# Kernel optimization log

Measured on AMD Instinct MI355X. Metric: run time of the kernel, lower is better.

Reference implementation:

```python
import jax, jax.numpy as jnp
import numpy as np

N = 100000; E = 200000; H = 64; P2 = 250000; P3 = 500000; G = 2048; NC = 10
NF = 18; EF = 18; Y = 0.25; EPS_BN = 1e-5


def setup_inputs() -> dict:
    key = jax.random.key(0)
    ks = jax.random.split(key, 20)
    def rn(i, shape, s=0.05):
        return jax.random.normal(ks[i], shape, jnp.float32) * s
    inp = {}
    inp["x"] = jax.random.normal(ks[0], (N, NF), jnp.float32)
    inp["edge_attr"] = jax.random.normal(ks[1], (E, EF), jnp.float32)
    inp["paths2"] = jax.random.randint(ks[2], (P2, 2), 0, N, jnp.int32)
    inp["ei2"] = jax.random.randint(ks[3], (P2, 1), 0, E, jnp.int32)
    inp["paths3"] = jax.random.randint(ks[4], (P3, 3), 0, N, jnp.int32)
    inp["ei3"] = jax.random.randint(ks[5], (P3, 2), 0, E, jnp.int32)
    inp["batch"] = jnp.sort(jax.random.randint(ks[6], (N,), 0, G, jnp.int32))
    inp["w_feat"] = rn(7, (NF, H)); inp["b_feat"] = jnp.zeros((H,), jnp.float32)
    inp["w_bond"] = rn(8, (EF, H)); inp["b_bond"] = jnp.zeros((H,), jnp.float32)
    inp["w_ih"] = rn(9, (4 * H, 2 * H)); inp["w_hh"] = rn(10, (4 * H, H))
    inp["b_ih"] = jnp.zeros((4 * H,), jnp.float32); inp["b_hh"] = jnp.zeros((4 * H,), jnp.float32)
    inp["bn_g"] = jnp.ones((2, H), jnp.float32); inp["bn_b"] = jnp.zeros((2, H), jnp.float32)
    inp["mlp_w1"] = rn(11, (2, H, H)); inp["mlp_b1"] = jnp.zeros((2, H), jnp.float32)
    inp["bn1_g"] = jnp.ones((2, H), jnp.float32); inp["bn1_b"] = jnp.zeros((2, H), jnp.float32)
    inp["mlp_w2"] = rn(12, (2, H, H)); inp["mlp_b2"] = jnp.zeros((2, H), jnp.float32)
    inp["bn2_g"] = jnp.ones((2, H), jnp.float32); inp["bn2_b"] = jnp.zeros((2, H), jnp.float32)
    inp["w_att"] = rn(13, (H,)); inp["b_att"] = jnp.zeros((1,), jnp.float32)
    inp["w_l1"] = rn(14, (H, H)); inp["b_l1"] = jnp.zeros((H,), jnp.float32)
    inp["w_l2"] = rn(15, (H, NC)); inp["b_l2"] = jnp.zeros((NC,), jnp.float32)
    return inp


def _batch_norm(x, g, b):
    # training-mode BN: biased batch statistics, eps=1e-5 (torch BatchNorm1d)
    m = x.mean(axis=0)
    v = x.var(axis=0)
    return (x - m) * jax.lax.rsqrt(v + EPS_BN) * g + b


def _lstm_final(x_seq, w_ih, w_hh, b_ih, b_hh):
    # x_seq: [P, L, 2H]; torch LSTM gate order i,f,g,o; return final hidden [P, H]
    P = x_seq.shape[0]
    Hd = w_hh.shape[1]
    def step(carry, xt):
        h, c = carry
        gates = xt @ w_ih.T + b_ih + h @ w_hh.T + b_hh
        i, f, g, o = jnp.split(gates, 4, axis=-1)
        c = jax.nn.sigmoid(f) * c + jax.nn.sigmoid(i) * jnp.tanh(g)
        h = jax.nn.sigmoid(o) * jnp.tanh(c)
        return (h, c), None
    h0 = jnp.zeros((P, Hd), x_seq.dtype)
    (h, _), _ = jax.lax.scan(step, (h0, h0), jnp.swapaxes(x_seq, 0, 1))
    return h


def _conv(i, x_in, ea_enc, paths, ei, w_ih, w_hh, b_ih, b_hh, bn_g, bn_b,
          mlp_w1, mlp_b1, bn1_g, bn1_b, mlp_w2, mlp_b2, bn2_g, bn2_b):
    P = paths.shape[0]
    ea = ea_enc[ei]                                        # [P, L-1, H]
    ea = jnp.concatenate([jnp.zeros((P, 1, H), ea.dtype), ea], axis=1)  # [P, L, H]
    x_cat = jnp.concatenate([x_in[paths], ea], axis=-1)    # [P, L, 2H]
    h = _lstm_final(x_cat, w_ih, w_hh, b_ih, b_hh)         # [P, H]
    h = jax.ops.segment_sum(h, paths[:, -1], num_segments=N)  # scatter_add to nodes
    h = _batch_norm(h, bn_g[i], bn_b[i])                   # residuals=False
    h = jax.nn.relu(_batch_norm(h @ mlp_w1[i] + mlp_b1[i], bn1_g[i], bn1_b[i]))
    h = jax.nn.relu(_batch_norm(h @ mlp_w2[i] + mlp_b2[i], bn2_g[i], bn2_b[i]))
    return h


def _attention(query, keys, w_att, b_att):
    scores = []
    for k in keys:
        s = jnp.sum(query * k, axis=0)                     # [H], sum over nodes
        s = (s - s.min()) / (s.max() - s.min() + 1e-6)
        scores.append(s @ w_att + b_att[0])                # scalar
    w = jax.nn.softmax(jnp.stack(scores))                  # [K]
    rep = sum(k * w[j] for j, k in enumerate(keys))
    return rep + query


def _forward(x, edge_attr, w_feat, b_feat, w_bond, b_bond, w_ih, w_hh, b_ih, b_hh,
             bn_g, bn_b, mlp_w1, mlp_b1, bn1_g, bn1_b, mlp_w2, mlp_b2, bn2_g, bn2_b,
             w_att, b_att, w_l1, b_l1, w_l2, b_l2, paths2, ei2, paths3, ei3, batch):
    W0 = x @ w_feat + b_feat                               # [N, H]
    ea_enc = edge_attr @ w_bond + b_bond                   # [E, H]
    common = (w_ih, w_hh, b_ih, b_hh, bn_g, bn_b, mlp_w1, mlp_b1, bn1_g, bn1_b,
              mlp_w2, mlp_b2, bn2_g, bn2_b)
    W1 = _conv(0, W0, ea_enc, paths2, ei2, *common)
    Win = (1.0 - Y) * W0 - Y * W1
    W2 = _conv(1, Win, ea_enc, paths3, ei3, *common)
    out = _attention(W0, [W1, W2], w_att, b_att)           # [N, H]
    out = jax.ops.segment_sum(out, batch, num_segments=G)  # global_add_pool -> [G, H]
    out = jax.nn.relu(out @ w_l1 + b_l1)
    return out @ w_l2 + b_l2                               # [G, NC]


def reference(x, edge_attr, paths2, ei2, paths3, ei3, batch, w_feat, b_feat,
              w_bond, b_bond, w_ih, w_hh, b_ih, b_hh, bn_g, bn_b, mlp_w1, mlp_b1,
              bn1_g, bn1_b, mlp_w2, mlp_b2, bn2_g, bn2_b, w_att, b_att,
              w_l1, b_l1, w_l2, b_l2):
    return _forward(x, edge_attr, w_feat, b_feat, w_bond, b_bond, w_ih, w_hh, b_ih, b_hh,
                    bn_g, bn_b, mlp_w1, mlp_b1, bn1_g, bn1_b, mlp_w2, mlp_b2, bn2_g, bn2_b,
                    w_att, b_att, w_l1, b_l1, w_l2, b_l2, paths2, ei2, paths3, ei3, batch)
```

## Files before the change

### kernel.cpp

```cpp
#include <hip/hip_runtime.h>
#include <math.h>

#define NNODES 100000
#define NEDGES 200000
#define HD 64
#define NP2 250000
#define NP3 500000
#define NG 2048
#define NCLS 10
#define NFEAT 18
#define EFEAT 18

typedef short short8v __attribute__((ext_vector_type(8)));
typedef float f32x4 __attribute__((ext_vector_type(4)));

__device__ __forceinline__ unsigned short bf16r(float a) {
    unsigned u = __builtin_bit_cast(unsigned, a);
    return (unsigned short)((u + 0x7FFFu + ((u >> 16) & 1u)) >> 16);
}

__global__ void prep_bias(const float* __restrict__ b_ih, const float* __restrict__ b_hh,
                          float* __restrict__ bsum) {
    int j = threadIdx.x;
    bsum[j] = b_ih[j] + b_hh[j];
}

__global__ void prep_bp(const float* __restrict__ w_ih, const float* __restrict__ w_hh,
                        unsigned short* __restrict__ Bp) {
    int gid = blockIdx.x * 256 + threadIdx.x;
    if (gid >= 6 * 16 * 64 * 8) return;
    int kc = gid >> 13;
    int rem = gid & 8191;
    int nt = rem >> 9;
    int rem2 = rem & 511;
    int l = rem2 >> 3, j = rem2 & 7;
    int c = l & 15, q = l >> 4;
    int jh = nt >> 2, qg = nt & 3;
    int k = kc * 32 + q * 8 + j;
    int n = qg * 64 + 16 * jh + c;
    float f = (k < 128) ? w_ih[n * 128 + k] : w_hh[n * 64 + (k - 128)];
    Bp[gid] = bf16r(f);
}

__global__ void encode_all(const float* __restrict__ X, const float* __restrict__ Wf,
                           const float* __restrict__ bf,
                           const float* __restrict__ Ea, const float* __restrict__ Wb,
                           const float* __restrict__ bb,
                           float* __restrict__ W0, unsigned short* __restrict__ W0b,
                           unsigned short* __restrict__ eab) {
    long gid = (long)blockIdx.x * 256 + threadIdx.x;
    if (gid >= (long)(NNODES + NEDGES) * 64) return;
    long r = gid >> 6;
    int col = (int)(gid & 63);
    if (r < NNODES) {
        float acc = bf[col];
        const float* xr = X + r * NFEAT;
        for (int k = 0; k < NFEAT; ++k) acc += xr[k] * Wf[k * 64 + col];
        W0[gid] = acc;
        W0b[gid] = bf16r(acc);
    } else {
        long r2 = r - NNODES;
        float acc = bb[col];
        const float* xr = Ea + r2 * EFEAT;
        for (int k = 0; k < EFEAT; ++k) acc += xr[k] * Wb[k * 64 + col];
        eab[r2 * 64 + col] = bf16r(acc);
    }
}

template <int L>
__global__ __launch_bounds__(256, 2)
void conv_mfma(const unsigned short* __restrict__ xb, const unsigned short* __restrict__ eab,
               const int* __restrict__ paths, const int* __restrict__ ei,
               const unsigned short* __restrict__ Bp, const float* __restrict__ bsum,
               float* __restrict__ hsum, int P) {
    __shared__ unsigned short Al[64 * 200];

    const int t = threadIdx.x;
    const int w = t >> 6, lane = t & 63;
    const int c = lane & 15, q = lane >> 4;
    const int pl = t >> 2, gq = t & 3;
    const long pg = (long)blockIdx.x * 64 + pl;
    const int pc = (pg < P) ? (int)pg : P - 1;

    short8v Bfr[6][4];
#pragma unroll
    for (int kc = 0; kc < 6; ++kc)
#pragma unroll
        for (int qg = 0; qg < 4; ++qg)
            Bfr[kc][qg] = *(const short8v*)&Bp[(((kc * 16) + (w * 4 + qg)) * 64 + lane) * 8];

    float breg[4];
#pragma unroll
    for (int qg = 0; qg < 4; ++qg) breg[qg] = bsum[qg * 64 + 16 * w + c];

    float creg[16];
#pragma unroll
    for (int i = 0; i < 16; ++i) creg[i] = 0.f;

    f32x4 acc[4][4];

    uint4 nu0, nu1, ev0, ev1;
    {
        int node = paths[pc * L + 0];
        const uint4* s4 = (const uint4*)(xb + (size_t)node * HD);
        nu0 = s4[2 * gq]; nu1 = s4[2 * gq + 1];
    }

    for (int step = 0; step < L; ++step) {
        *(uint4*)&Al[pl * 200 + gq * 16] = nu0;
        *(uint4*)&Al[pl * 200 + gq * 16 + 8] = nu1;
        if (step > 0) {
            *(uint4*)&Al[pl * 200 + 64 + gq * 16] = ev0;
            *(uint4*)&Al[pl * 200 + 64 + gq * 16 + 8] = ev1;
        }
#pragma unroll
        for (int mt = 0; mt < 4; ++mt)
#pragma unroll
            for (int qg = 0; qg < 4; ++qg) {
                f32x4 v; v[0] = breg[qg]; v[1] = breg[qg]; v[2] = breg[qg]; v[3] = breg[qg];
                acc[mt][qg] = v;
            }
        __syncthreads();

        if (step + 1 < L) {
            int node = paths[pc * L + step + 1];
            const uint4* s4 = (const uint4*)(xb + (size_t)node * HD);
            nu0 = s4[2 * gq]; nu1 = s4[2 * gq + 1];
            int e = ei[pc * (L - 1) + step];
            const uint4* e4 = (const uint4*)(eab + (size_t)e * HD);
            ev0 = e4[2 * gq]; ev1 = e4[2 * gq + 1];
        }

#define CHUNK(KC)                                                              \
        {                                                                      \
            _Pragma("unroll")                                                  \
            for (int mt = 0; mt < 4; ++mt) {                                   \
                short8v af = *(const short8v*)&Al[(mt * 16 + c) * 200 + (KC) * 32 + q * 8]; \
                _Pragma("unroll")                                              \
                for (int qg = 0; qg < 4; ++qg)                                 \
                    acc[mt][qg] = __builtin_amdgcn_mfma_f32_16x16x32_bf16(     \
                        af, Bfr[KC][qg], acc[mt][qg], 0, 0, 0);                \
            }                                                                  \
        }
        if (step == 0) {
            CHUNK(0) CHUNK(1)
        } else {
            CHUNK(0) CHUNK(1) CHUNK(2) CHUNK(3) CHUNK(4) CHUNK(5)
        }
#undef CHUNK
        __syncthreads();

#pragma unroll
        for (int mt = 0; mt < 4; ++mt) {
#pragma unroll
            for (int r = 0; r < 4; ++r) {
                float gi = acc[mt][0][r], gf = acc[mt][1][r];
                float gg = acc[mt][2][r], go = acc[mt][3][r];
                float ea = __expf(-gf), eb = __expf(-gi);
                float ed = __expf(-2.f * gg), eo = __expf(-go);
                float pa = 1.f + ea, pb = 1.f + eb, pd = 1.f + ed;
                float cn = (creg[mt * 4 + r] * pb * pd + (1.f - ed) * pa) *
                           __builtin_amdgcn_rcpf(pa * pb * pd);
                creg[mt * 4 + r] = cn;
                float et = __expf(-2.f * cn);
                float hn = (1.f - et) *
                           __builtin_amdgcn_rcpf((1.f + eo) * (1.f + et));
                if (step < L - 1) {
                    Al[(mt * 16 + q * 4 + r) * 200 + 128 + 16 * w + c] = bf16r(hn);
                } else {
                    long pr = (long)blockIdx.x * 64 + mt * 16 + q * 4 + r;
                    if (pr < P) {
                        int node = paths[pr * L + (L - 1)];
                        atomicAdd(hsum + (size_t)node * HD + 16 * w + c, hn);
                    }
                }
            }
        }
    }
}

__global__ void col_stats(const float* __restrict__ X, int nrows, float* __restrict__ out) {
    int col = threadIdx.x & 63, rg = threadIdx.x >> 6;
    float s = 0.f, q = 0.f;
    long stride = (long)gridDim.x * 4;
    for (long r = (long)blockIdx.x * 4 + rg; r < nrows; r += stride) {
        float v = X[r * 64 + col];
        s += v;
        q += v * v;
    }
    __shared__ float red[2][256];
    red[0][threadIdx.x] = s;
    red[1][threadIdx.x] = q;
    __syncthreads();
    if (threadIdx.x < 64) {
        int c = threadIdx.x;
        float ss = red[0][c] + red[0][c + 64] + red[0][c + 128] + red[0][c + 192];
        float qq = red[1][c] + red[1][c + 64] + red[1][c + 128] + red[1][c + 192];
        atomicAdd(out + c, ss);
        atomicAdd(out + 64 + c, qq);
    }
}

__device__ __forceinline__ void bn_affine(const float* stats, const float* g,
                                          const float* b, int col, int nrows,
                                          float& a, float& c) {
    float inv = 1.0f / (float)nrows;
    float mean = stats[col] * inv;
    float var = stats[64 + col] * inv - mean * mean;
    a = g[col] * rsqrtf(var + 1e-5f);
    c = b[col] - mean * a;
}

template <bool INRELU, bool STATS>
__global__ __launch_bounds__(256)
void gemm64(const float* __restrict__ X, const float* __restrict__ stats_in,
            const float* __restrict__ bn_gm, const float* __restrict__ bn_bt,
            const float* __restrict__ W, const float* __restrict__ bias,
            float* __restrict__ Y, float* stats, int nrows) {
    __shared__ float Xs[64 * 64];
    __shared__ float red[2][256];
    const int t = threadIdx.x;
    const int col = t & 63, rg = t >> 6;
    const long r0 = (long)blockIdx.x * 64;

    float a = 1.f, c = 0.f;
    if (stats_in) bn_affine(stats_in, bn_gm, bn_bt, col, nrows, a, c);

    for (int i = 0; i < 16; ++i) {
        int rl = rg * 16 + i;
        long r = r0 + rl;
        float v = (r < nrows) ? X[r * 64 + col] : 0.f;
        v = v * a + c;
        if (INRELU) v = fmaxf(v, 0.f);
        Xs[rl * 64 + col] = v;
    }
    __syncthreads();

    float wreg[64];
#pragma unroll
    for (int k = 0; k < 64; ++k) wreg[k] = W[k * 64 + col];
    float bs = bias[col];
    float ssum = 0.f, ssq = 0.f;

    for (int i = 0; i < 16; ++i) {
        int rl = rg * 16 + i;
        long r = r0 + rl;
        const float4* xs4 = (const float4*)(Xs + rl * 64);
        float acc = bs;
#pragma unroll
        for (int k4 = 0; k4 < 16; ++k4) {
            float4 xv = xs4[k4];
            acc += xv.x * wreg[4 * k4] + xv.y * wreg[4 * k4 + 1] +
                   xv.z * wreg[4 * k4 + 2] + xv.w * wreg[4 * k4 + 3];
        }
        if (r < nrows) {
            Y[r * 64 + col] = acc;
            ssum += acc;
            ssq += acc * acc;
        }
    }
    if (STATS) {
        red[0][t] = ssum;
        red[1][t] = ssq;
        __syncthreads();
        if (t < 64) {
            float s = red[0][t] + red[0][t + 64] + red[0][t + 128] + red[0][t + 192];
            float qq = red[1][t] + red[1][t + 64] + red[1][t + 128] + red[1][t + 192];
            atomicAdd(stats + t, s);
            atomicAdd(stats + 64 + t, qq);
        }
    }
}

__global__ void bn_apply1(float* __restrict__ W1, const float* __restrict__ stats,
                          const float* __restrict__ g, const float* __restrict__ b,
                          const float* __restrict__ W0, unsigned short* __restrict__ Winb,
                          long n) {
    long gid = (long)blockIdx.x * 256 + threadIdx.x;
    if (gid >= n * 64) return;
    int col = (int)(gid & 63);
    float a, c;
    bn_affine(stats, g, b, col, (int)n, a, c);
    float v = fmaxf(W1[gid] * a + c, 0.f);
    W1[gid] = v;
    Winb[gid] = bf16r(0.75f * W0[gid] - 0.25f * v);
}

__global__ void bn_apply_att(float* __restrict__ W2, const float* __restrict__ stats,
                             const float* __restrict__ g, const float* __restrict__ b,
                             const float* __restrict__ W0, const float* __restrict__ W1,
                             float* __restrict__ atts, int n) {
    int col = threadIdx.x & 63, rg = threadIdx.x >> 6;
    float a, c;
    bn_affine(stats, g, b, col, n, a, c);
    float s1 = 0.f, s2 = 0.f;
    long stride = (long)gridDim.x * 4;
    for (long r = (long)blockIdx.x * 4 + rg; r < n; r += stride) {
        long gid = r * 64 + col;
        float v = fmaxf(W2[gid] * a + c, 0.f);
        W2[gid] = v;
        float q0 = W0[gid];
        s1 += q0 * W1[gid];
        s2 += q0 * v;
    }
    __shared__ float red[2][256];
    red[0][threadIdx.x] = s1;
    red[1][threadIdx.x] = s2;
    __syncthreads();
    if (threadIdx.x < 64) {
        int cc = threadIdx.x;
        float a1 = red[0][cc] + red[0][cc + 64] + red[0][cc + 128] + red[0][cc + 192];
        float a2 = red[1][cc] + red[1][cc + 64] + red[1][cc + 128] + red[1][cc + 192];
        atomicAdd(atts + cc, a1);
        atomicAdd(atts + 64 + cc, a2);
    }
}

__global__ void att_softmax(const float* __restrict__ atts, const float* __restrict__ w_att,
                            const float* __restrict__ b_att, float* __restrict__ watt) {
    int h = threadIdx.x;
    float z[2];
    for (int k = 0; k < 2; ++k) {
        float s = atts[64 * k + h];
        float mn = s, mx = s;
        for (int off = 32; off > 0; off >>= 1) {
            mn = fminf(mn, __shfl_down(mn, off));
            mx = fmaxf(mx, __shfl_down(mx, off));
        }
        mn = __shfl(mn, 0);
        mx = __shfl(mx, 0);
        float sn = (s - mn) / (mx - mn + 1e-6f);
        float d = sn * w_att[h];
        for (int off = 32; off > 0; off >>= 1) d += __shfl_down(d, off);
        z[k] = __shfl(d, 0) + b_att[0];
    }
    if (h == 0) {
        float m = fmaxf(z[0], z[1]);
        float e0 = expf(z[0] - m), e1 = expf(z[1] - m);
        float inv = 1.0f / (e0 + e1);
        watt[0] = e0 * inv;
        watt[1] = e1 * inv;
    }
}

#define PROWS 128
__global__ void pool_rep(const float* __restrict__ W0, const float* __restrict__ W1,
                         const float* __restrict__ W2, const float* __restrict__ watt,
                         const int* __restrict__ batch, float* __restrict__ pooled, int n) {
    int col = threadIdx.x & 63, rg = threadIdx.x >> 6;
    long r0 = (long)blockIdx.x * PROWS;
    float w1 = watt[0], w2 = watt[1];
    float acc = 0.f;
    int curg = -1;
    for (int i = rg; i < PROWS; i += 4) {
        long r = r0 + i;
        if (r >= n) break;
        int g = batch[r];
        long gid = r * 64 + col;
        float rep = W0[gid] + w1 * W1[gid] + w2 * W2[gid];
        if (g != curg) {
            if (curg >= 0) atomicAdd(pooled + (size_t)curg * 64 + col, acc);
            curg = g;
            acc = 0.f;
        }
        acc += rep;
    }
    if (curg >= 0) atomicAdd(pooled + (size_t)curg * 64 + col, acc);
}

__global__ __launch_bounds__(256)
void head_kernel(const float* __restrict__ pooled, const float* __restrict__ w_l1,
                 const float* __restrict__ b_l1, const float* __restrict__ w_l2,
                 const float* __restrict__ b_l2, float* __restrict__ out) {
    __shared__ float Xs[64 * 64];
    __shared__ float Ys[64 * 65];
    const int t = threadIdx.x;
    const int col = t & 63, rg = t >> 6;
    const int r0 = blockIdx.x * 64;

    for (int i = 0; i < 16; ++i) {
        int rl = rg * 16 + i;
        Xs[rl * 64 + col] = fmaxf(pooled[(size_t)(r0 + rl) * 64 + col], 0.f);
    }
    __syncthreads();

    float wreg[64];
#pragma unroll
    for (int k = 0; k < 64; ++k) wreg[k] = w_l1[k * 64 + col];
    float bs = b_l1[col];

    for (int i = 0; i < 16; ++i) {
        int rl = rg * 16 + i;
        const float4* xs4 = (const float4*)(Xs + rl * 64);
        float acc = bs;
#pragma unroll
        for (int k4 = 0; k4 < 16; ++k4) {
            float4 xv = xs4[k4];
            acc += xv.x * wreg[4 * k4] + xv.y * wreg[4 * k4 + 1] +
                   xv.z * wreg[4 * k4 + 2] + xv.w * wreg[4 * k4 + 3];
        }
        Ys[rl * 65 + col] = fmaxf(acc, 0.f);
    }
    __syncthreads();

    for (int idx = t; idx < 64 * NCLS; idx += 256) {
        int row = idx / NCLS, j = idx - row * NCLS;
        float acc = b_l2[j];
#pragma unroll
        for (int k = 0; k < 64; ++k) acc += Ys[row * 65 + k] * w_l2[k * NCLS + j];
        out[(size_t)(r0 + row) * NCLS + j] = acc;
    }
}

extern "C" void kernel_launch(void* const* d_in, const int* in_sizes, int n_in,
                              void* d_out, int out_size, void* d_ws, size_t ws_size,
                              hipStream_t stream) {
    const float* x         = (const float*)d_in[0];
    const float* edge_attr = (const float*)d_in[1];
    const int*   paths2    = (const int*)d_in[2];
    const int*   ei2       = (const int*)d_in[3];
    const int*   paths3    = (const int*)d_in[4];
    const int*   ei3       = (const int*)d_in[5];
    const int*   batch     = (const int*)d_in[6];
    const float* w_feat    = (const float*)d_in[7];
    const float* b_feat    = (const float*)d_in[8];
    const float* w_bond    = (const float*)d_in[9];
    const float* b_bond    = (const float*)d_in[10];
    const float* w_ih      = (const float*)d_in[11];
    const float* w_hh      = (const float*)d_in[12];
    const float* b_ih      = (const float*)d_in[13];
    const float* b_hh      = (const float*)d_in[14];
    const float* bn_g      = (const float*)d_in[15];
    const float* bn_b      = (const float*)d_in[16];
    const float* mlp_w1    = (const float*)d_in[17];
    const float* mlp_b1    = (const float*)d_in[18];
    const float* bn1_g     = (const float*)d_in[19];
    const float* bn1_b     = (const float*)d_in[20];
    const float* mlp_w2    = (const float*)d_in[21];
    const float* mlp_b2    = (const float*)d_in[22];
    const float* bn2_g     = (const float*)d_in[23];
    const float* bn2_b     = (const float*)d_in[24];
    const float* w_att     = (const float*)d_in[25];
    const float* b_att     = (const float*)d_in[26];
    const float* w_l1      = (const float*)d_in[27];
    const float* b_l1      = (const float*)d_in[28];
    const float* w_l2      = (const float*)d_in[29];
    const float* b_l2      = (const float*)d_in[30];

    const size_t N64 = (size_t)NNODES * 64;
    float* ws = (float*)d_ws;
    float* W0     = ws;
    float* W1     = W0 + N64;
    float* W2     = W1 + N64;
    float* Wtmp   = W2 + N64;
    float* hsum1  = Wtmp + N64;
    float* hsum2  = hsum1 + N64;
    unsigned short* W0b  = (unsigned short*)(hsum2 + N64);
    unsigned short* Winb = W0b + N64;
    unsigned short* eab  = Winb + N64;
    unsigned short* Bp   = eab + (size_t)NEDGES * 64;
    float* bsum   = (float*)(Bp + 6 * 16 * 64 * 8);
    float* st     = bsum + 256;
    float* atts   = st + 6 * 128;
    float* watt   = atts + 128;
    float* pooled = watt + 64;

    hipMemsetAsync(st, 0, (6 * 128 + 128 + 64) * sizeof(float), stream);
    hipMemsetAsync(pooled, 0, (size_t)NG * 64 * sizeof(float), stream);
    hipMemsetAsync(hsum1, 0, 2 * N64 * sizeof(float), stream);

    prep_bias<<<1, 256, 0, stream>>>(b_ih, b_hh, bsum);
    prep_bp<<<192, 256, 0, stream>>>(w_ih, w_hh, Bp);
    encode_all<<<(int)(((size_t)(NNODES + NEDGES) * 64 + 255) / 256), 256, 0, stream>>>(
        x, w_feat, b_feat, edge_attr, w_bond, b_bond, W0, W0b, eab);

    conv_mfma<2><<<(NP2 + 63) / 64, 256, 0, stream>>>(W0b, eab, paths2, ei2, Bp, bsum, hsum1, NP2);

    col_stats<<<1024, 256, 0, stream>>>(hsum1, NNODES, st + 0);
    gemm64<false, true><<<(NNODES + 63) / 64, 256, 0, stream>>>(hsum1, st + 0, bn_g + 0, bn_b + 0, mlp_w1, mlp_b1, Wtmp, st + 128, NNODES);
    gemm64<true, true><<<(NNODES + 63) / 64, 256, 0, stream>>>(Wtmp, st + 128, bn1_g + 0, bn1_b + 0, mlp_w2, mlp_b2, W1, st + 256, NNODES);
    bn_apply1<<<(NNODES * 64 + 255) / 256, 256, 0, stream>>>(W1, st + 256, bn2_g + 0, bn2_b + 0, W0, Winb, NNODES);

    conv_mfma<3><<<(NP3 + 63) / 64, 256, 0, stream>>>(Winb, eab, paths3, ei3, Bp, bsum, hsum2, NP3);

    col_stats<<<1024, 256, 0, stream>>>(hsum2, NNODES, st + 384);
    gemm64<false, true><<<(NNODES + 63) / 64, 256, 0, stream>>>(hsum2, st + 384, bn_g + 64, bn_b + 64, mlp_w1 + 4096, mlp_b1 + 64, Wtmp, st + 512, NNODES);
    gemm64<true, true><<<(NNODES + 63) / 64, 256, 0, stream>>>(Wtmp, st + 512, bn1_g + 64, bn1_b + 64, mlp_w2 + 4096, mlp_b2 + 64, W2, st + 640, NNODES);
    bn_apply_att<<<1024, 256, 0, stream>>>(W2, st + 640, bn2_g + 64, bn2_b + 64, W0, W1, atts, NNODES);

    att_softmax<<<1, 64, 0, stream>>>(atts, w_att, b_att, watt);
    pool_rep<<<(NNODES + PROWS - 1) / PROWS, 256, 0, stream>>>(W0, W1, W2, watt, batch, pooled, NNODES);
    head_kernel<<<NG / 64, 256, 0, stream>>>(pooled, w_l1, b_l1, w_l2, b_l2, (float*)d_out);
}
```

Before: 787.0 us.

## Double-buffer LSTM LDS tile, stream weight fragments, fold log2e into weights

The conv LSTM kernel now reloads B weight fragments from global/L2 in rotating 3-chunk register buffers instead of keeping all 24 fragments resident. This lowers register pressure so the launch bound can rise from 2 to 3 waves per SIMD. The LDS A tile is double-buffered, which removes one __syncthreads per step, and the gathers for the next step are issued in the middle of the MFMA chain. The gate weights and biases are pre-scaled by log2e (2*log2e for the g gate), so the activations use exp2 directly instead of __expf. The cost is repeated weight loads every step and twice the LDS per block, which could limit occupancy.

```diff
diff --git a/kernel.cpp b/kernel.cpp
--- a/kernel.cpp
+++ b/kernel.cpp
@@ -19,10 +19,13 @@
     return (unsigned short)((u + 0x7FFFu + ((u >> 16) & 1u)) >> 16);
 }
 
+#define LOG2E 1.4426950408889634f
+
 __global__ void prep_bias(const float* __restrict__ b_ih, const float* __restrict__ b_hh,
                           float* __restrict__ bsum) {
     int j = threadIdx.x;
-    bsum[j] = b_ih[j] + b_hh[j];
+    float s = ((j >> 6) == 2) ? 2.f * LOG2E : LOG2E;
+    bsum[j] = (b_ih[j] + b_hh[j]) * s;
 }
 
 __global__ void prep_bp(const float* __restrict__ w_ih, const float* __restrict__ w_hh,
@@ -39,7 +42,8 @@
     int k = kc * 32 + q * 8 + j;
     int n = qg * 64 + 16 * jh + c;
     float f = (k < 128) ? w_ih[n * 128 + k] : w_hh[n * 64 + (k - 128)];
-    Bp[gid] = bf16r(f);
+    float s = (qg == 2) ? 2.f * LOG2E : LOG2E;
+    Bp[gid] = bf16r(f * s);
 }
 
 __global__ void encode_all(const float* __restrict__ X, const float* __restrict__ Wf,
@@ -68,12 +72,12 @@
 }
 
 template <int L>
-__global__ __launch_bounds__(256, 2)
+__global__ __launch_bounds__(256, 3)
 void conv_mfma(const unsigned short* __restrict__ xb, const unsigned short* __restrict__ eab,
                const int* __restrict__ paths, const int* __restrict__ ei,
                const unsigned short* __restrict__ Bp, const float* __restrict__ bsum,
                float* __restrict__ hsum, int P) {
-    __shared__ unsigned short Al[64 * 200];
+    __shared__ unsigned short Al[2][64 * 200];
 
     const int t = threadIdx.x;
     const int w = t >> 6, lane = t & 63;
@@ -82,73 +86,92 @@
     const long pg = (long)blockIdx.x * 64 + pl;
     const int pc = (pg < P) ? (int)pg : P - 1;
 
-    short8v Bfr[6][4];
-#pragma unroll
-    for (int kc = 0; kc < 6; ++kc)
-#pragma unroll
-        for (int qg = 0; qg < 4; ++qg)
-            Bfr[kc][qg] = *(const short8v*)&Bp[(((kc * 16) + (w * 4 + qg)) * 64 + lane) * 8];
+    const short8v* __restrict__ Bv = (const short8v*)Bp;
+    const int bbase = (w * 4) * 64 + lane;
 
     float breg[4];
 #pragma unroll
-    for (int qg = 0; qg < 4; ++qg) breg[qg] = bsum[qg * 64 + 16 * w + c];
+    for (int g2 = 0; g2 < 4; ++g2) breg[g2] = bsum[g2 * 64 + 16 * w + c];
 
     float creg[16];
 #pragma unroll
     for (int i = 0; i < 16; ++i) creg[i] = 0.f;
 
     f32x4 acc[4][4];
-
+    short8v bs0[4], bs1[4], bs2[4];
     uint4 nu0, nu1, ev0, ev1;
+
     {
         int node = paths[pc * L + 0];
         const uint4* s4 = (const uint4*)(xb + (size_t)node * HD);
-        nu0 = s4[2 * gq]; nu1 = s4[2 * gq + 1];
-    }
-
+        uint4 a0 = s4[2 * gq], a1 = s4[2 * gq + 1];
+        *(uint4*)&Al[0][pl * 200 + gq * 16] = a0;
+        *(uint4*)&Al[0][pl * 200 + gq * 16 + 8] = a1;
+    }
+    __syncthreads();
+
+    int cur = 0;
     for (int step = 0; step < L; ++step) {
-        *(uint4*)&Al[pl * 200 + gq * 16] = nu0;
-        *(uint4*)&Al[pl * 200 + gq * 16 + 8] = nu1;
-        if (step > 0) {
-            *(uint4*)&Al[pl * 200 + 64 + gq * 16] = ev0;
-            *(uint4*)&Al[pl * 200 + 64 + gq * 16 + 8] = ev1;
-        }
+        const unsigned short* Ac = Al[cur];
+        unsigned short* An = Al[cur ^ 1];
+
 #pragma unroll
         for (int mt = 0; mt < 4; ++mt)
 #pragma unroll
-            for (int qg = 0; qg < 4; ++qg) {
-                f32x4 v; v[0] = breg[qg]; v[1] = breg[qg]; v[2] = breg[qg]; v[3] = breg[qg];
-                acc[mt][qg] = v;
+            for (int g2 = 0; g2 < 4; ++g2) {
+                f32x4 v; v[0] = breg[g2]; v[1] = breg[g2]; v[2] = breg[g2]; v[3] = breg[g2];
+                acc[mt][g2] = v;
             }
-        __syncthreads();
-
-        if (step + 1 < L) {
-            int node = paths[pc * L + step + 1];
-            const uint4* s4 = (const uint4*)(xb + (size_t)node * HD);
-            nu0 = s4[2 * gq]; nu1 = s4[2 * gq + 1];
-            int e = ei[pc * (L - 1) + step];
-            const uint4* e4 = (const uint4*)(eab + (size_t)e * HD);
-            ev0 = e4[2 * gq]; ev1 = e4[2 * gq + 1];
-        }
-
-#define CHUNK(KC)                                                              \
-        {                                                                      \
-            _Pragma("unroll")                                                  \
-            for (int mt = 0; mt < 4; ++mt) {                                   \
-                short8v af = *(const short8v*)&Al[(mt * 16 + c) * 200 + (KC) * 32 + q * 8]; \
-                _Pragma("unroll")                                              \
-                for (int qg = 0; qg < 4; ++qg)                                 \
-                    acc[mt][qg] = __builtin_amdgcn_mfma_f32_16x16x32_bf16(     \
-                        af, Bfr[KC][qg], acc[mt][qg], 0, 0, 0);                \
-            }                                                                  \
-        }
+
+#define LOADB(BUF, KC)                                                         \
+        { _Pragma("unroll")                                                    \
+          for (int g2 = 0; g2 < 4; ++g2)                                       \
+              BUF[g2] = Bv[(KC) * 1024 + g2 * 64 + bbase]; }
+
+#define CHUNKS(BUF, KC)                                                        \
+        { _Pragma("unroll")                                                    \
+          for (int mt = 0; mt < 4; ++mt) {                                     \
+              short8v af = *(const short8v*)&Ac[(mt * 16 + c) * 200 + (KC) * 32 + q * 8]; \
+              _Pragma("unroll")                                                \
+              for (int g2 = 0; g2 < 4; ++g2)                                   \
+                  acc[mt][g2] = __builtin_amdgcn_mfma_f32_16x16x32_bf16(       \
+                      af, BUF[g2], acc[mt][g2], 0, 0, 0);                      \
+          } }
+
         if (step == 0) {
-            CHUNK(0) CHUNK(1)
+            LOADB(bs0, 0)
+            LOADB(bs1, 1)
+            {
+                int node = paths[pc * L + 1];
+                const uint4* s4 = (const uint4*)(xb + (size_t)node * HD);
+                nu0 = s4[2 * gq]; nu1 = s4[2 * gq + 1];
+                int e = ei[pc * (L - 1) + 0];
+                const uint4* e4 = (const uint4*)(eab + (size_t)e * HD);
+                ev0 = e4[2 * gq]; ev1 = e4[2 * gq + 1];
+            }
+            CHUNKS(bs0, 0)
+            CHUNKS(bs1, 1)
         } else {
-            CHUNK(0) CHUNK(1) CHUNK(2) CHUNK(3) CHUNK(4) CHUNK(5)
-        }
-#undef CHUNK
-        __syncthreads();
+            LOADB(bs0, 0)
+            LOADB(bs1, 1)
+            LOADB(bs2, 2)
+            CHUNKS(bs0, 0) LOADB(bs0, 3)
+            CHUNKS(bs1, 1) LOADB(bs1, 4)
+            CHUNKS(bs2, 2) LOADB(bs2, 5)
+            if (step + 1 < L) {
+                int node = paths[pc * L + step + 1];
+                const uint4* s4 = (const uint4*)(xb + (size_t)node * HD);
+                nu0 = s4[2 * gq]; nu1 = s4[2 * gq + 1];
+                int e = ei[pc * (L - 1) + step];
+                const uint4* e4 = (const uint4*)(eab + (size_t)e * HD);
+                ev0 = e4[2 * gq]; ev1 = e4[2 * gq + 1];
+            }
+            CHUNKS(bs0, 3)
+            CHUNKS(bs1, 4)
+            CHUNKS(bs2, 5)
+        }
+#undef LOADB
+#undef CHUNKS
 
 #pragma unroll
         for (int mt = 0; mt < 4; ++mt) {
@@ -156,17 +179,19 @@
             for (int r = 0; r < 4; ++r) {
                 float gi = acc[mt][0][r], gf = acc[mt][1][r];
                 float gg = acc[mt][2][r], go = acc[mt][3][r];
-                float ea = __expf(-gf), eb = __expf(-gi);
-                float ed = __expf(-2.f * gg), eo = __expf(-go);
+                float ea = __builtin_amdgcn_exp2f(-gf);
+                float eb = __builtin_amdgcn_exp2f(-gi);
+                float ed = __builtin_amdgcn_exp2f(-gg);
+                float eo = __builtin_amdgcn_exp2f(-go);
                 float pa = 1.f + ea, pb = 1.f + eb, pd = 1.f + ed;
                 float cn = (creg[mt * 4 + r] * pb * pd + (1.f - ed) * pa) *
                            __builtin_amdgcn_rcpf(pa * pb * pd);
                 creg[mt * 4 + r] = cn;
-                float et = __expf(-2.f * cn);
+                float et = __builtin_amdgcn_exp2f(-2.8853900817779268f * cn);
                 float hn = (1.f - et) *
                            __builtin_amdgcn_rcpf((1.f + eo) * (1.f + et));
                 if (step < L - 1) {
-                    Al[(mt * 16 + q * 4 + r) * 200 + 128 + 16 * w + c] = bf16r(hn);
+                    An[(mt * 16 + q * 4 + r) * 200 + 128 + 16 * w + c] = bf16r(hn);
                 } else {
                     long pr = (long)blockIdx.x * 64 + mt * 16 + q * 4 + r;
                     if (pr < P) {
@@ -176,6 +201,15 @@
                 }
             }
         }
+
+        if (step + 1 < L) {
+            *(uint4*)&An[pl * 200 + gq * 16] = nu0;
+            *(uint4*)&An[pl * 200 + gq * 16 + 8] = nu1;
+            *(uint4*)&An[pl * 200 + 64 + gq * 16] = ev0;
+            *(uint4*)&An[pl * 200 + 64 + gq * 16 + 8] = ev1;
+            __syncthreads();
+        }
+        cur ^= 1;
     }
 }
 
```

After: 775.1 us. About the same (-1.5%).
